# Optimization experiments

Measured on AMD Instinct MI355X. Metric: run time of the kernel, lower is better.

## Reference

```python
import jax, jax.numpy as jnp
import numpy as np
from jax import lax

NEG_INF = -1e30  # finite stand-in for -inf (keeps grads clean)
BLANK = 6624


def setup_inputs() -> dict:
    key = jax.random.key(0)
    k1, k2 = jax.random.split(key)
    B, T, C, L = 32, 512, 6625, 32
    log_probs = jax.random.normal(k1, (B, T, C), dtype=jnp.float32)
    targets = jax.random.randint(k2, (B, L), 0, BLANK, dtype=jnp.int32)  # labels exclude blank
    input_lengths = jnp.full((B,), T, dtype=jnp.int32)
    target_lengths = jnp.full((B,), L, dtype=jnp.int32)
    return {"log_probs": log_probs, "targets": targets,
            "input_lengths": input_lengths, "target_lengths": target_lengths}


def _ctc_loss(lp, targets, input_lengths, target_lengths, blank):
    # lp: [B, T, C] (already log-normalized as in the source), targets: [B, L]
    B, T, C = lp.shape
    L = targets.shape[1]
    S = 2 * L + 1
    # extended label sequence: blank, t0, blank, t1, ..., tL-1, blank  -> [B, S]
    ext = jnp.full((B, S), blank, dtype=targets.dtype)
    ext = ext.at[:, 1::2].set(targets)
    ext_m2 = jnp.pad(ext, ((0, 0), (2, 0)), constant_values=blank)[:, :S]
    allow_skip = (ext != blank) & (ext != ext_m2)  # [B, S]

    lp_tbc = jnp.transpose(lp, (1, 0, 2))  # [T, B, C]
    # emission log-prob of each extended label at each time: [T, B, S]
    emit = jnp.take_along_axis(lp_tbc, jnp.broadcast_to(ext[None], (T, B, S)), axis=2)

    alpha0 = jnp.full((B, S), NEG_INF, dtype=lp.dtype)
    alpha0 = alpha0.at[:, 0].set(emit[0, :, 0])
    alpha0 = alpha0.at[:, 1].set(emit[0, :, 1])

    pad1 = jnp.full((B, 1), NEG_INF, dtype=lp.dtype)
    pad2 = jnp.full((B, 2), NEG_INF, dtype=lp.dtype)

    def step(alpha, inp):
        emit_t, t = inp
        a1 = jnp.concatenate([pad1, alpha[:, :-1]], axis=1)
        a2 = jnp.concatenate([pad2, alpha[:, :-2]], axis=1)
        a2 = jnp.where(allow_skip, a2, NEG_INF)
        new = jnp.logaddexp(jnp.logaddexp(alpha, a1), a2) + emit_t
        new = jnp.where((t < input_lengths)[:, None], new, alpha)  # freeze past input_length
        return new, None

    alpha_T, _ = lax.scan(step, alpha0, (emit[1:], jnp.arange(1, T)))

    idx1 = (2 * target_lengths).astype(jnp.int32)            # final blank
    idx2 = jnp.maximum(2 * target_lengths - 1, 0).astype(jnp.int32)  # final label
    l1 = jnp.take_along_axis(alpha_T, idx1[:, None], axis=1)[:, 0]
    l2 = jnp.take_along_axis(alpha_T, idx2[:, None], axis=1)[:, 0]
    loss = -jnp.logaddexp(l1, l2)  # [B]
    # zero_infinity=True: infinite losses -> 0
    loss = jnp.where(loss > 1e20, 0.0, loss)
    # reduction='mean' (torch semantics: divide by target_length, then mean)
    return (loss / jnp.maximum(target_lengths, 1).astype(loss.dtype)).mean()


def reference(log_probs, targets, input_lengths, target_lengths):
    # Faithful to source: log_softmax over dim=1 (the TIME axis of [B, T, C])
    lp = jax.nn.log_softmax(log_probs, axis=1)
    return _ctc_loss(lp, targets, input_lengths, target_lengths, BLANK)
```

## Files before the change

kernel.cpp:

```cpp
#include <hip/hip_runtime.h>

#define NEG_INF -1e30f

constexpr int BLANKC = 6624;
constexpr int NCLS   = 6625;
constexpr int TT     = 512;
constexpr int LL     = 32;
constexpr int NSLOT  = LL + 1;
constexpr int BB     = 32;
constexpr int KPT    = TT / 64;

constexpr float L2E = 1.44269504088896340736f;
constexpr float LN2 = 0.693147180559945309417f;

__device__ __forceinline__ float fast_exp2(float x) {
#if __has_builtin(__builtin_amdgcn_exp2f)
    return __builtin_amdgcn_exp2f(x);
#else
    return exp2f(x);
#endif
}
__device__ __forceinline__ float fast_log2(float x) {
#if __has_builtin(__builtin_amdgcn_logf)
    return __builtin_amdgcn_logf(x);
#else
    return log2f(x);
#endif
}

__device__ __forceinline__ float dpp_shr1(float x) {
#if __has_builtin(__builtin_amdgcn_update_dpp)
    return __int_as_float(__builtin_amdgcn_update_dpp(
        __float_as_int(NEG_INF), __float_as_int(x),
        0x138 , 0xF, 0xF, false));
#else
    float r = __shfl_up(x, 1, 64);
    if ((int)(threadIdx.x & 63) == 0) r = NEG_INF;
    return r;
#endif
}

__device__ __forceinline__ float wave_allmax(float v) {
#pragma unroll
    for (int off = 32; off > 0; off >>= 1)
        v = fmaxf(v, __shfl_xor(v, off, 64));
    return v;
}
__device__ __forceinline__ float wave_allsum(float v) {
#pragma unroll
    for (int off = 32; off > 0; off >>= 1)
        v += __shfl_xor(v, off, 64);
    return v;
}

__global__ __launch_bounds__(256) void ctc_colnorm(
    const float* __restrict__ x,
    const int*   __restrict__ targets,
    float*       __restrict__ cols)
{
    const int wid  = blockIdx.x * 4 + (threadIdx.x >> 6);
    const int lane = threadIdx.x & 63;
    if (wid >= BB * NSLOT) return;
    const int b    = wid / NSLOT;
    const int slot = wid - b * NSLOT;
    const int c    = (slot == 0) ? BLANKC : targets[b * LL + slot - 1];

    const float* xb = x + (size_t)b * TT * NCLS + c;
    float v[KPT];
    float m = NEG_INF;
#pragma unroll
    for (int k = 0; k < KPT; ++k) {
        v[k] = xb[(size_t)(lane + 64 * k) * NCLS];
        m = fmaxf(m, v[k]);
    }
    m = wave_allmax(m);
    float w[KPT];
    float s = 0.f;
#pragma unroll
    for (int k = 0; k < KPT; ++k) {
        w[k] = (v[k] - m) * L2E;
        s += fast_exp2(w[k]);
    }
    s = wave_allsum(s);
    const float ls = fast_log2(s);

    float* cb = cols + (size_t)(b * NSLOT + slot) * TT;
#pragma unroll
    for (int k = 0; k < KPT; ++k) cb[lane + 64 * k] = w[k] - ls;
}

__device__ __forceinline__ void ctc_step(float& alpha, float& a64,
                                         float e, float eb, bool allow) {
    float am1 = dpp_shr1(alpha);
    float am2 = dpp_shr1(am1);
    am2 = allow ? am2 : NEG_INF;
    const float aold = alpha;
    const float m  = fmaxf(fmaxf(aold, am1), am2);
    const float r  = fast_exp2(aold - m) + fast_exp2(am1 - m) + fast_exp2(am2 - m);
    const float na = m + fast_log2(r) + e;
    const float m2   = fmaxf(a64, aold);
    const float r2   = fast_exp2(a64 - m2) + fast_exp2(aold - m2);
    const float na64 = m2 + fast_log2(r2) + eb;
    alpha = na;
    a64   = na64;
}

#define LOADC(E, c) do {                                                      \
    const float4* __p = reinterpret_cast<const float4*>(ec + ((c) << 5));     \
    _Pragma("unroll")                                                         \
    for (int k = 0; k < 8; ++k) {                                             \
        float4 __t = __p[k];                                                  \
        E[4*k+0] = __t.x; E[4*k+1] = __t.y;                                   \
        E[4*k+2] = __t.z; E[4*k+3] = __t.w;                                   \
    }                                                                         \
} while (0)

#define CHUNK(E, u0) do {                                                     \
    _Pragma("unroll")                                                         \
    for (int u = (u0); u < 32; ++u) {                                         \
        const float e_  = E[u];                                               \
        const float eb_ = __int_as_float(                                     \
            __builtin_amdgcn_readfirstlane(__float_as_int(E[u])));            \
        ctc_step(alpha, a64, e_, eb_, allow);                                 \
    }                                                                         \
} while (0)

__global__ __launch_bounds__(64) void ctc_alpha(
    const float* __restrict__ cols,
    const int*   __restrict__ targets,
    const int*   __restrict__ input_lengths,
    const int*   __restrict__ target_lengths,
    float*       __restrict__ part)
{
    const int b = blockIdx.x;
    const int s = threadIdx.x;
    const int j = s >> 1;
    const bool odd = (s & 1) != 0;

    const int ext_s = odd ? targets[b * LL + j] : BLANKC;
    const bool allow = odd && (ext_s != BLANKC) &&
                       (s == 1 || ext_s != targets[b * LL + j - 1]);

    const float* ec = cols + ((size_t)b * NSLOT + (odd ? (size_t)(1 + j) : (size_t)0)) * TT;

    const int ilen = input_lengths[b];
    const int tlen = target_lengths[b];
    const int nsteps = min(ilen, TT);

    float alpha;
    float a64 = NEG_INF;

    if (nsteps == TT) {
        float eA[32], eB[32];
        LOADC(eA, 0);
        LOADC(eB, 1);
        alpha = (s < 2) ? eA[0] : NEG_INF;
        CHUNK(eA, 1);
#pragma unroll 1
        for (int p = 1; p + 1 < 16; p += 2) {
            LOADC(eA, p + 1);
            CHUNK(eB, 0);
            LOADC(eB, p + 2);
            CHUNK(eA, 0);
        }
        CHUNK(eB, 0);
    } else {
        const float* bc = cols + (size_t)b * NSLOT * TT;
        alpha = (s < 2) ? ec[0] : NEG_INF;
        for (int t = 1; t < nsteps; ++t) {
            const float e  = ec[t];
            const float eb = bc[t];
            ctc_step(alpha, a64, e, eb, allow);
        }
    }

    const int idx1 = 2 * tlen;
    const int idx2 = max(2 * tlen - 1, 0);
    const float l1 = (idx1 >= 64) ? __shfl(a64, 63, 64) : __shfl(alpha, idx1, 64);
    const float l2 = __shfl(alpha, idx2, 64);
    const float mm = fmaxf(l1, l2);
    const float res2 = mm + fast_log2(fast_exp2(l1 - mm) + fast_exp2(l2 - mm));
    float loss = -LN2 * res2;
    if (loss > 1e20f) loss = 0.f;
    loss /= (float)max(tlen, 1);
    if (s == 0) part[b] = loss;
}

__global__ __launch_bounds__(64) void ctc_reduce(
    const float* __restrict__ part, float* __restrict__ out)
{
    const int lane = threadIdx.x;
    float v = (lane < BB) ? part[lane] : 0.f;
#pragma unroll
    for (int off = 32; off > 0; off >>= 1) v += __shfl_xor(v, off, 64);
    if (lane == 0) out[0] = v / (float)BB;
}

extern "C" void kernel_launch(void* const* d_in, const int* in_sizes, int n_in,
                              void* d_out, int out_size, void* d_ws, size_t ws_size,
                              hipStream_t stream) {
    const float* lp      = (const float*)d_in[0];
    const int*   targets = (const int*)d_in[1];
    const int*   ilen    = (const int*)d_in[2];
    const int*   tlen    = (const int*)d_in[3];
    float* out = (float*)d_out;

    constexpr size_t COLS_ELEMS = (size_t)BB * NSLOT * TT;
    float* cols = (float*)d_ws;
    float* part = (float*)d_ws + COLS_ELEMS;

    const int gridA = (BB * NSLOT + 3) / 4;
    ctc_colnorm<<<gridA, 256, 0, stream>>>(lp, targets, cols);
    ctc_alpha<<<BB, 64, 0, stream>>>(cols, targets, ilen, tlen, part);
    ctc_reduce<<<1, 64, 0, stream>>>(part, out);
}
```

Baseline: 518.4 us.

## Fuse column normalization and CTC alpha recursion into one block per batch

Merges the column log-softmax kernel and the alpha-recursion kernel into a single 512-thread block per batch item. Label columns are staged in rotated shared memory, and the blank column goes through a small global scratch read back by the same wave. This removes a kernel launch and the global round trip of the normalized columns. The cost is that only 32 blocks gather the strided inputs, compared with 264 waves across many blocks before, so memory-level parallelism in the gather phase drops sharply.

Result: slower. 541.9 us (+4.5%).

```diff
diff --git a/kernel.cpp b/kernel.cpp
--- a/kernel.cpp
+++ b/kernel.cpp
@@ -6,9 +6,7 @@
 constexpr int NCLS   = 6625;
 constexpr int TT     = 512;
 constexpr int LL     = 32;
-constexpr int NSLOT  = LL + 1;
 constexpr int BB     = 32;
-constexpr int KPT    = TT / 64;
 
 constexpr float L2E = 1.44269504088896340736f;
 constexpr float LN2 = 0.693147180559945309417f;
@@ -51,42 +49,6 @@
     for (int off = 32; off > 0; off >>= 1)
         v += __shfl_xor(v, off, 64);
     return v;
-}
-
-__global__ __launch_bounds__(256) void ctc_colnorm(
-    const float* __restrict__ x,
-    const int*   __restrict__ targets,
-    float*       __restrict__ cols)
-{
-    const int wid  = blockIdx.x * 4 + (threadIdx.x >> 6);
-    const int lane = threadIdx.x & 63;
-    if (wid >= BB * NSLOT) return;
-    const int b    = wid / NSLOT;
-    const int slot = wid - b * NSLOT;
-    const int c    = (slot == 0) ? BLANKC : targets[b * LL + slot - 1];
-
-    const float* xb = x + (size_t)b * TT * NCLS + c;
-    float v[KPT];
-    float m = NEG_INF;
-#pragma unroll
-    for (int k = 0; k < KPT; ++k) {
-        v[k] = xb[(size_t)(lane + 64 * k) * NCLS];
-        m = fmaxf(m, v[k]);
-    }
-    m = wave_allmax(m);
-    float w[KPT];
-    float s = 0.f;
-#pragma unroll
-    for (int k = 0; k < KPT; ++k) {
-        w[k] = (v[k] - m) * L2E;
-        s += fast_exp2(w[k]);
-    }
-    s = wave_allsum(s);
-    const float ls = fast_log2(s);
-
-    float* cb = cols + (size_t)(b * NSLOT + slot) * TT;
-#pragma unroll
-    for (int k = 0; k < KPT; ++k) cb[lane + 64 * k] = w[k] - ls;
 }
 
 __device__ __forceinline__ void ctc_step(float& alpha, float& a64,
@@ -105,71 +67,139 @@
     a64   = na64;
 }
 
-#define LOADC(E, c) do {                                                      \
-    const float4* __p = reinterpret_cast<const float4*>(ec + ((c) << 5));     \
+__global__ __launch_bounds__(512) void ctc_fused(
+    const float* __restrict__ x,
+    const int*   __restrict__ targets,
+    const int*   __restrict__ input_lengths,
+    const int*   __restrict__ target_lengths,
+    float*       __restrict__ gblank,
+    float*       __restrict__ part)
+{
+    __shared__ float lcols[LL * TT];
+
+    const int b    = blockIdx.x;
+    const int wave = threadIdx.x >> 6;
+    const int lane = threadIdx.x & 63;
+    const float* xb = x + (size_t)b * TT * NCLS;
+    float* gb = gblank + (size_t)b * TT;
+
+    int cls[4];
+#pragma unroll
+    for (int i = 0; i < 4; ++i) cls[i] = targets[b * LL + (wave * 4 + i)];
+
+    float vB[8];
+    if (wave == 0) {
+#pragma unroll
+        for (int k = 0; k < 8; ++k)
+            vB[k] = xb[(size_t)(lane + 64 * k) * NCLS + BLANKC];
+    }
+    float vL[4][8];
+#pragma unroll
+    for (int i = 0; i < 4; ++i) {
+#pragma unroll
+        for (int k = 0; k < 8; ++k)
+            vL[i][k] = xb[(size_t)(lane + 64 * k) * NCLS + cls[i]];
+    }
+#pragma unroll
+    for (int i = 0; i < 4; ++i) {
+        const int col = wave * 4 + i;
+        float m = NEG_INF;
+#pragma unroll
+        for (int k = 0; k < 8; ++k) m = fmaxf(m, vL[i][k]);
+        m = wave_allmax(m);
+        float w8[8];
+        float s = 0.f;
+#pragma unroll
+        for (int k = 0; k < 8; ++k) { w8[k] = (vL[i][k] - m) * L2E; s += fast_exp2(w8[k]); }
+        s = wave_allsum(s);
+        const float ls = fast_log2(s);
+#pragma unroll
+        for (int k = 0; k < 8; ++k) {
+            const int t = lane + 64 * k;
+            lcols[col * TT + ((t + col) & (TT - 1))] = w8[k] - ls;
+        }
+    }
+    float bl[8];
+    if (wave == 0) {
+        float m = NEG_INF;
+#pragma unroll
+        for (int k = 0; k < 8; ++k) m = fmaxf(m, vB[k]);
+        m = wave_allmax(m);
+        float s = 0.f;
+#pragma unroll
+        for (int k = 0; k < 8; ++k) { bl[k] = (vB[k] - m) * L2E; s += fast_exp2(bl[k]); }
+        s = wave_allsum(s);
+        const float ls = fast_log2(s);
+#pragma unroll
+        for (int k = 0; k < 8; ++k) { bl[k] -= ls; gb[lane + 64 * k] = bl[k]; }
+    }
+    __syncthreads();
+    if (wave != 0) return;
+
+    const int s    = lane;
+    const int j    = s >> 1;
+    const bool odd = (s & 1) != 0;
+    const int colj = j;
+    const int cbase = colj * TT;
+
+    const int tj = odd ? targets[b * LL + j] : BLANKC;
+    const bool allow = odd && (tj != BLANKC) &&
+                       (s == 1 || tj != targets[b * LL + j - 1]);
+
+    const int ilen = input_lengths[b];
+    const int tlen = target_lengths[b];
+    const int nsteps = min(ilen, TT);
+
+#define LOADE(E, c) do {                                                      \
+    _Pragma("unroll")                                                         \
+    for (int u = 0; u < 32; ++u) {                                            \
+        const int t_ = ((c) << 5) + u;                                        \
+        E[u] = lcols[cbase + ((t_ + colj) & (TT - 1))];                       \
+    }                                                                         \
+} while (0)
+
+#define LOADB(EBV, c) do {                                                    \
+    const float4* __p = reinterpret_cast<const float4*>(gb + ((c) << 5));     \
     _Pragma("unroll")                                                         \
     for (int k = 0; k < 8; ++k) {                                             \
         float4 __t = __p[k];                                                  \
-        E[4*k+0] = __t.x; E[4*k+1] = __t.y;                                   \
-        E[4*k+2] = __t.z; E[4*k+3] = __t.w;                                   \
+        EBV[4*k+0] = __t.x; EBV[4*k+1] = __t.y;                               \
+        EBV[4*k+2] = __t.z; EBV[4*k+3] = __t.w;                               \
     }                                                                         \
 } while (0)
 
-#define CHUNK(E, u0) do {                                                     \
+#define CHUNKF(E, EBV, u0) do {                                               \
     _Pragma("unroll")                                                         \
     for (int u = (u0); u < 32; ++u) {                                         \
-        const float e_  = E[u];                                               \
-        const float eb_ = __int_as_float(                                     \
-            __builtin_amdgcn_readfirstlane(__float_as_int(E[u])));            \
+        const float eb_ = EBV[u];                                             \
+        const float e_  = odd ? E[u] : eb_;                                   \
         ctc_step(alpha, a64, e_, eb_, allow);                                 \
     }                                                                         \
 } while (0)
 
-__global__ __launch_bounds__(64) void ctc_alpha(
-    const float* __restrict__ cols,
-    const int*   __restrict__ targets,
-    const int*   __restrict__ input_lengths,
-    const int*   __restrict__ target_lengths,
-    float*       __restrict__ part)
-{
-    const int b = blockIdx.x;
-    const int s = threadIdx.x;
-    const int j = s >> 1;
-    const bool odd = (s & 1) != 0;
-
-    const int ext_s = odd ? targets[b * LL + j] : BLANKC;
-    const bool allow = odd && (ext_s != BLANKC) &&
-                       (s == 1 || ext_s != targets[b * LL + j - 1]);
-
-    const float* ec = cols + ((size_t)b * NSLOT + (odd ? (size_t)(1 + j) : (size_t)0)) * TT;
-
-    const int ilen = input_lengths[b];
-    const int tlen = target_lengths[b];
-    const int nsteps = min(ilen, TT);
-
     float alpha;
     float a64 = NEG_INF;
 
     if (nsteps == TT) {
-        float eA[32], eB[32];
-        LOADC(eA, 0);
-        LOADC(eB, 1);
-        alpha = (s < 2) ? eA[0] : NEG_INF;
-        CHUNK(eA, 1);
+        float eA[32], eB[32], bA[32], bBuf[32];
+        LOADE(eA, 0); LOADB(bA, 0);
+        LOADE(eB, 1); LOADB(bBuf, 1);
+        alpha = (s < 2) ? (odd ? eA[0] : bA[0]) : NEG_INF;
+        CHUNKF(eA, bA, 1);
 #pragma unroll 1
         for (int p = 1; p + 1 < 16; p += 2) {
-            LOADC(eA, p + 1);
-            CHUNK(eB, 0);
-            LOADC(eB, p + 2);
-            CHUNK(eA, 0);
+            LOADE(eA, p + 1); LOADB(bA, p + 1);
+            CHUNKF(eB, bBuf, 0);
+            LOADE(eB, p + 2); LOADB(bBuf, p + 2);
+            CHUNKF(eA, bA, 0);
         }
-        CHUNK(eB, 0);
+        CHUNKF(eB, bBuf, 0);
     } else {
-        const float* bc = cols + (size_t)b * NSLOT * TT;
-        alpha = (s < 2) ? ec[0] : NEG_INF;
+        const float eb0 = gb[0];
+        alpha = (s < 2) ? (odd ? lcols[cbase + (colj & (TT - 1))] : eb0) : NEG_INF;
         for (int t = 1; t < nsteps; ++t) {
-            const float e  = ec[t];
-            const float eb = bc[t];
+            const float eb = gb[t];
+            const float e  = odd ? lcols[cbase + ((t + colj) & (TT - 1))] : eb;
             ctc_step(alpha, a64, e, eb, allow);
         }
     }
@@ -184,6 +214,10 @@
     if (loss > 1e20f) loss = 0.f;
     loss /= (float)max(tlen, 1);
     if (s == 0) part[b] = loss;
+
+#undef LOADE
+#undef LOADB
+#undef CHUNKF
 }
 
 __global__ __launch_bounds__(64) void ctc_reduce(
@@ -205,12 +239,9 @@
     const int*   tlen    = (const int*)d_in[3];
     float* out = (float*)d_out;
 
-    constexpr size_t COLS_ELEMS = (size_t)BB * NSLOT * TT;
-    float* cols = (float*)d_ws;
-    float* part = (float*)d_ws + COLS_ELEMS;
-
-    const int gridA = (BB * NSLOT + 3) / 4;
-    ctc_colnorm<<<gridA, 256, 0, stream>>>(lp, targets, cols);
-    ctc_alpha<<<BB, 64, 0, stream>>>(cols, targets, ilen, tlen, part);
+    float* gblank = (float*)d_ws;
+    float* part   = (float*)d_ws + (size_t)BB * TT;
+
+    ctc_fused<<<BB, 512, 0, stream>>>(lp, targets, ilen, tlen, gblank, part);
     ctc_reduce<<<1, 64, 0, stream>>>(part, out);
 }
```
